# Performance work log

Hardware: AMD Instinct MI355X
Metric: run time of the kernel (lower is better)

The kernel has to match this reference:

```python
import jax, jax.numpy as jnp
import numpy as np
from jax import lax

# Conv4d decomposed (as in the torch implementation) into a sum of Conv3d's
# over the first spatial kernel axis. Each 3D conv is vectorized by folding
# the strided first-dim slices into the batch dimension.

def conv4d(x, w, b, stride=(2, 2, 2, 2), padding=(1, 1, 1, 1)):
    # x: [B, Ci, D1, D2, D3, D4]; w: [Co, Ci, K1, K2, K3, K4]; b: [Co]
    B, Ci, D1, D2, D3, D4 = x.shape
    Co, _, K1, K2, K3, K4 = w.shape
    s1, p1 = stride[0], padding[0]
    T = (D1 + 2 * p1 - K1) // s1 + 1  # output size along first spatial dim
    xp = jnp.pad(x, ((0, 0), (0, 0), (p1, p1), (0, 0), (0, 0), (0, 0)))
    pad3 = [(padding[j], padding[j]) for j in (1, 2, 3)]
    out = None
    for i in range(K1):  # small fixed loop over kernel taps along dim0
        xi = xp[:, :, i:i + s1 * (T - 1) + 1:s1]           # [B, Ci, T, D2, D3, D4]
        xi = jnp.moveaxis(xi, 2, 1).reshape(B * T, Ci, D2, D3, D4)
        yi = lax.conv_general_dilated(
            xi, w[:, :, i], window_strides=stride[1:], padding=pad3,
            dimension_numbers=('NCDHW', 'OIDHW', 'NCDHW'))
        out = yi if out is None else out + yi
    O2, O3, O4 = out.shape[2], out.shape[3], out.shape[4]
    out = out.reshape(B, T, Co, O2, O3, O4)
    out = jnp.moveaxis(out, 1, 2)                          # [B, Co, T, O2, O3, O4]
    return out + b[None, :, None, None, None, None]


def setup_inputs() -> dict:
    key = jax.random.key(0)
    k0, k1, k2, k3, k4 = jax.random.split(key, 5)
    C, R = 16, 4  # in_channel, mlp_ratio
    H = C * R     # 64
    x = jax.random.normal(k0, (1, C, 32, 32, 32, 32), dtype=jnp.float32)
    w1 = jax.random.normal(k1, (H, C, 3, 3, 3, 3), dtype=jnp.float32) * 0.02
    b1 = jax.random.normal(k2, (H,), dtype=jnp.float32) * 0.02
    w2 = jax.random.normal(k3, (C, H, 3, 3, 3, 3), dtype=jnp.float32) * 0.02
    b2 = jax.random.normal(k4, (C,), dtype=jnp.float32) * 0.02
    return {'x': x, 'w1': w1, 'b1': b1, 'w2': w2, 'b2': b2}


def reference(x, w1, b1, w2, b2):
    h = conv4d(x, w1, b1)                      # [1, 64, 16, 16, 16, 16]
    h = jax.nn.gelu(h, approximate=False)      # exact erf GELU (torch default)
    return conv4d(h, w2, b2)                   # [1, 16, 8, 8, 8, 8]
```

## Files before the change

kernel.cpp:

```cpp
#include <hip/hip_runtime.h>
#include <hip/hip_bf16.h>
#include <math.h>


typedef __attribute__((ext_vector_type(8))) short short8;
typedef __attribute__((ext_vector_type(4))) float f32x4;
typedef __attribute__((ext_vector_type(4))) unsigned int uint4v;

__device__ __forceinline__ unsigned short f2bf(float v) {
    __hip_bfloat16 b = __float2bfloat16(v);
    return *(unsigned short*)&b;
}

__global__ void setup_kernel(const float* __restrict__ w1, const float* __restrict__ w2,
                             const float* __restrict__ b2,
                             unsigned short* __restrict__ w1p, unsigned short* __restrict__ w2p,
                             uint4v* __restrict__ hz, float* __restrict__ out) {
    int b = blockIdx.x, tid = threadIdx.x;
    if (b < 544) {
        int i = b * 256 + tid;
        int kp = i % 136, co = (i / 136) & 63, ci = i / 8704;
        float v = 0.f;
        if (kp < 108 && (kp & 3) < 3) v = w1[(co * 16 + ci) * 81 + (kp >> 2) * 3 + (kp & 3)];
        w1p[i] = f2bf(v);
    } else if (b < 1088) {
        int i = (b - 544) * 256 + tid;
        int kp = i % 136, co = (i / 136) & 15, ci = i / 2176;
        float v = 0.f;
        if (kp < 108 && (kp & 3) < 3) v = w2[(co * 64 + ci) * 81 + (kp >> 2) * 3 + (kp & 3)];
        w2p[i] = f2bf(v);
    } else if (b < 1344) {
        int i = (b - 1088) * 256 + tid;
        out[i] = b2[i >> 12];
    } else {
        int i = (b - 1344) * 256 + tid;
        hz[i] = (uint4v){0, 0, 0, 0};
        int j = i + 704512;
        if (j < 839808) hz[j] = (uint4v){0, 0, 0, 0};
    }
}

__global__ __launch_bounds__(256) void conv1_mfma(
        const float* __restrict__ x, const unsigned short* __restrict__ w1p,
        const float* __restrict__ b1, unsigned short* __restrict__ hpad) {
    __shared__ unsigned short sX[36000];

    const int tid = threadIdx.x;
    const int bid = blockIdx.x;
    const int t4 = bid & 1, t3 = (bid >> 1) & 7, t2 = (bid >> 4) & 7, t1 = bid >> 7;
    const int bo1 = 2 * t1, bo2 = 2 * t2, bo3 = 2 * t3, bo4 = 8 * t4;
    const int g1b = 2 * bo1 - 1, g2b = 2 * bo2 - 1, g3b = 2 * bo3 - 1, g4b = 2 * bo4 - 1;

    int offs[5], swb[5];
    unsigned mka = 0, mkb = 0;
#pragma unroll
    for (int r = 0; r < 5; ++r) {
        int u = tid + 256 * r;
        bool uok = u < 1125;
        int uu = uok ? u : 0;
        int p = uu % 9, q = uu / 9;
        int i3 = q % 5; q /= 5;
        int i2 = q % 5; int i1 = q / 5;
        int g1 = g1b + i1, g2 = g2b + i2, g3 = g3b + i3;
        bool ok123 = uok & ((unsigned)g1 < 32u) & ((unsigned)g2 < 32u) & ((unsigned)g3 < 32u);
        int g4a = g4b + 2 * p;
        offs[r] = ((g1 * 32 + g2) * 32 + g3) * 32 + g4a;
        if (ok123 && (unsigned)g4a < 32u) mka |= 1u << r;
        if (ok123 && (unsigned)(g4a + 1) < 32u) mkb |= 1u << r;
        swb[r] = 2 * (((i1 * 5 + i2) * 5 + i3) * 18 + 2 * p);
    }

    auto gatherX = [&](int ci, float (&a)[5], float (&b)[5]) {
        const float* xc = x + (size_t)ci * 1048576;
#pragma unroll
        for (int r = 0; r < 5; ++r) {
            float va = 0.f, vb = 0.f;
            if ((mka >> r) & 1) va = xc[offs[r]];
            if ((mkb >> r) & 1) vb = xc[offs[r] + 1];
            a[r] = va; b[r] = vb;
        }
    };
    auto writeSlab = [&](int ci, const float (&a)[5], const float (&b)[5]) {
        char* slab = (char*)sX + ci * 4500;
#pragma unroll
        for (int r = 0; r < 4; ++r)
            *(unsigned*)(slab + swb[r]) = (unsigned)f2bf(a[r]) | ((unsigned)f2bf(b[r]) << 16);
        if (tid < 101)
            *(unsigned*)(slab + swb[4]) = (unsigned)f2bf(a[4]) | ((unsigned)f2bf(b[4]) << 16);
    };

    {
        float a0[5], b0[5], a1[5], b1v[5];
        gatherX(0, a0, b0);
        gatherX(1, a1, b1v);
        for (int cc = 0; cc < 16; cc += 2) {
            writeSlab(cc, a0, b0);
            if (cc + 2 < 16) gatherX(cc + 2, a0, b0);
            writeSlab(cc + 1, a1, b1v);
            if (cc + 3 < 16) gatherX(cc + 3, a1, b1v);
        }
    }
    __syncthreads();

    const int lane = tid & 63, wv = tid >> 6;
    const int n16 = lane & 15, hi = lane >> 4;
    const int ct0 = 2 * (wv & 1);
    const int st0 = 2 * (wv >> 1);

    int fpb[2];
#pragma unroll
    for (int tt = 0; tt < 2; ++tt) {
        int sp = (st0 + tt) * 16 + n16;
        int o4l = sp & 7, o3l = (sp >> 3) & 1, o2l = (sp >> 4) & 1, o1l = sp >> 5;
        fpb[tt] = 2 * (900 * o1l + 180 * o2l + 36 * o3l + 2 * o4l);
    }
    int kof[4][2];
#pragma unroll
    for (int ks = 0; ks < 4; ++ks)
#pragma unroll
    for (int j = 0; j < 2; ++j) {
        int g = 8 * ks + 2 * hi + j;
        if (g > 26) g = 26;
        int k1 = g / 9, k2 = (g / 3) % 3, k3 = g % 3;
        kof[ks][j] = 2 * (450 * k1 + 90 * k2 + 18 * k3);
    }

    auto loadA = [&](int ci, short8 (&Ac)[8]) {
        const unsigned short* aw0 = w1p + (size_t)(ci * 64 + 16 * ct0 + n16) * 136 + hi * 8;
#pragma unroll
        for (int k = 0; k < 4; ++k) Ac[k] = *(const short8*)(aw0 + 32 * k);
        const unsigned short* aw1 = aw0 + 16 * 136;
#pragma unroll
        for (int k = 0; k < 4; ++k) Ac[4 + k] = *(const short8*)(aw1 + 32 * k);
    };
    auto readFR = [&](int ci, short8 (&fr)[2][4]) {
        const char* sx = (const char*)sX + ci * 4500;
#pragma unroll
        for (int tt = 0; tt < 2; ++tt) {
            const char* base = sx + fpb[tt];
#pragma unroll
            for (int ks = 0; ks < 4; ++ks) {
                unsigned r0 = *(const unsigned*)(base + kof[ks][0]);
                unsigned r1 = *(const unsigned*)(base + kof[ks][0] + 4);
                unsigned r2 = *(const unsigned*)(base + kof[ks][1]);
                unsigned r3 = *(const unsigned*)(base + kof[ks][1] + 4);
                uint4v t = (uint4v){r0, r1, r2, r3};
                fr[tt][ks] = *(short8*)&t;
            }
        }
    };

    f32x4 acc[2][2];
#pragma unroll
    for (int c = 0; c < 2; ++c)
#pragma unroll
    for (int t = 0; t < 2; ++t) acc[c][t] = (f32x4){0.f, 0.f, 0.f, 0.f};

    auto mfma16 = [&](const short8 (&Ac)[8], const short8 (&fr)[2][4]) {
        __builtin_amdgcn_s_setprio(1);
#pragma unroll
        for (int tt = 0; tt < 2; ++tt)
#pragma unroll
        for (int ks = 0; ks < 4; ++ks) {
            acc[0][tt] = __builtin_amdgcn_mfma_f32_16x16x32_bf16(Ac[ks],     fr[tt][ks], acc[0][tt], 0, 0, 0);
            acc[1][tt] = __builtin_amdgcn_mfma_f32_16x16x32_bf16(Ac[4 + ks], fr[tt][ks], acc[1][tt], 0, 0, 0);
        }
        __builtin_amdgcn_s_setprio(0);
    };

    short8 A0[8], A1[8], F0[2][4], F1[2][4];
    loadA(0, A0);
    loadA(1, A1);
    readFR(0, F0);

    for (int cc = 0; cc < 16; cc += 2) {
        readFR(cc + 1, F1);
        mfma16(A0, F0);
        if (cc < 14) { loadA(cc + 2, A0); readFR(cc + 2, F0); }
        mfma16(A1, F1);
        if (cc < 14) loadA(cc + 3, A1);
    }

#pragma unroll
    for (int c = 0; c < 2; ++c) {
#pragma unroll
        for (int tt = 0; tt < 2; ++tt) {
            int spl = 16 * (st0 + tt) + n16;
            int e4 = spl & 7, e3 = (spl >> 3) & 1, e2 = (spl >> 4) & 1, e1 = spl >> 5;
            size_t base = (size_t)(bo1 + e1 + 1) * 5832 + (bo2 + e2 + 1) * 324 +
                          (bo3 + e3 + 1) * 18 + (bo4 + e4 + 1);
#pragma unroll
            for (int r = 0; r < 4; ++r) {
                int co = 16 * (ct0 + c) + 4 * hi + r;
                float v = acc[c][tt][r] + b1[co];
                v = 0.5f * v * (1.f + erff(v * 0.70710678118654752f));
                hpad[(size_t)co * 104976 + base] = f2bf(v);
            }
        }
    }
}

__global__ __launch_bounds__(256) void conv2_mfma(
        const unsigned short* __restrict__ hpad, const unsigned short* __restrict__ w2p,
        float* __restrict__ out) {
    __shared__ unsigned short sX[18000];

    const int tid = threadIdx.x;
    const int bid = blockIdx.x;
    const int s = bid & 63, cig = bid >> 6;
    const int t3 = s & 3, t2 = (s >> 2) & 3, t1 = s >> 4;
    const int bo1 = 2 * t1, bo2 = 2 * t2, bo3 = 2 * t3;

    int offs[5], swb[5];
#pragma unroll
    for (int r = 0; r < 5; ++r) {
        int u = tid + 256 * r;
        if (u >= 1125) u = 0;
        int p = u % 9, q = u / 9;
        int i3 = q % 5; q /= 5;
        int i2 = q % 5; int i1 = q / 5;
        offs[r] = (2 * bo1 + i1) * 5832 + (2 * bo2 + i2) * 324 + (2 * bo3 + i3) * 18 + 2 * p;
        swb[r] = 2 * (((i1 * 5 + i2) * 5 + i3) * 18 + 2 * p);
    }

    {
        unsigned fa[5], na[5];
        const unsigned short* h0 = hpad + (size_t)(cig * 8) * 104976;
#pragma unroll
        for (int r = 0; r < 5; ++r) fa[r] = *(const unsigned*)(h0 + offs[r]);
        for (int s8 = 0; s8 < 8; ++s8) {
            if (s8 < 7) {
                const unsigned short* hc = hpad + (size_t)(cig * 8 + s8 + 1) * 104976;
#pragma unroll
                for (int r = 0; r < 5; ++r) na[r] = *(const unsigned*)(hc + offs[r]);
            }
            char* slab = (char*)sX + s8 * 4500;
#pragma unroll
            for (int r = 0; r < 4; ++r) *(unsigned*)(slab + swb[r]) = fa[r];
            if (tid < 101) *(unsigned*)(slab + swb[4]) = fa[4];
            if (s8 < 7) {
#pragma unroll
                for (int r = 0; r < 5; ++r) fa[r] = na[r];
            }
        }
    }
    __syncthreads();

    const int lane = tid & 63, wv = tid >> 6;
    const int n16 = lane & 15, hi = lane >> 4;

    int fpb;
    {
        int sp = wv * 16 + n16;
        int o4l = sp & 7, o3l = (sp >> 3) & 1, o2l = (sp >> 4) & 1, o1l = sp >> 5;
        fpb = 2 * (900 * o1l + 180 * o2l + 36 * o3l + 2 * o4l);
    }
    int kof[4][2];
#pragma unroll
    for (int ks = 0; ks < 4; ++ks)
#pragma unroll
    for (int j = 0; j < 2; ++j) {
        int g = 8 * ks + 2 * hi + j;
        if (g > 26) g = 26;
        int k1 = g / 9, k2 = (g / 3) % 3, k3 = g % 3;
        kof[ks][j] = 2 * (450 * k1 + 90 * k2 + 18 * k3);
    }

    auto loadA = [&](int s8, short8 (&Ac)[4]) {
        const unsigned short* aw = w2p + (size_t)((cig * 8 + s8) * 16 + n16) * 136 + hi * 8;
#pragma unroll
        for (int k = 0; k < 4; ++k) Ac[k] = *(const short8*)(aw + 32 * k);
    };
    auto readFR = [&](int s8, short8 (&fr)[4]) {
        const char* base = (const char*)sX + s8 * 4500 + fpb;
#pragma unroll
        for (int ks = 0; ks < 4; ++ks) {
            unsigned r0 = *(const unsigned*)(base + kof[ks][0]);
            unsigned r1 = *(const unsigned*)(base + kof[ks][0] + 4);
            unsigned r2 = *(const unsigned*)(base + kof[ks][1]);
            unsigned r3 = *(const unsigned*)(base + kof[ks][1] + 4);
            uint4v tmp = (uint4v){r0, r1, r2, r3};
            fr[ks] = *(short8*)&tmp;
        }
    };

    f32x4 acc = (f32x4){0.f, 0.f, 0.f, 0.f};
    short8 A0[4], A1[4], F0[4], F1[4];
    loadA(0, A0);
    loadA(1, A1);
    readFR(0, F0);

    auto mfma4 = [&](const short8 (&Ac)[4], const short8 (&fr)[4]) {
        __builtin_amdgcn_s_setprio(1);
#pragma unroll
        for (int ks = 0; ks < 4; ++ks)
            acc = __builtin_amdgcn_mfma_f32_16x16x32_bf16(Ac[ks], fr[ks], acc, 0, 0, 0);
        __builtin_amdgcn_s_setprio(0);
    };

    for (int cc = 0; cc < 8; cc += 2) {
        readFR(cc + 1, F1);
        mfma4(A0, F0);
        if (cc < 6) { loadA(cc + 2, A0); readFR(cc + 2, F0); }
        mfma4(A1, F1);
        if (cc < 6) loadA(cc + 3, A1);
    }

    {
        int spl = 16 * wv + n16;
        int e4 = spl & 7, e3 = (spl >> 3) & 1, e2 = (spl >> 4) & 1, e1 = spl >> 5;
        int o1 = bo1 + e1, o2 = bo2 + e2, o3 = bo3 + e3, o4 = e4;
#pragma unroll
        for (int r = 0; r < 4; ++r) {
            int co = 4 * hi + r;
            atomicAdd(&out[(size_t)co * 4096 + o1 * 512 + o2 * 64 + o3 * 8 + o4], acc[r]);
        }
    }
}

extern "C" void kernel_launch(void* const* d_in, const int* in_sizes, int n_in,
                              void* d_out, int out_size, void* d_ws, size_t ws_size,
                              hipStream_t stream) {
    const float* x  = (const float*)d_in[0];
    const float* w1 = (const float*)d_in[1];
    const float* b1 = (const float*)d_in[2];
    const float* w2 = (const float*)d_in[3];
    const float* b2 = (const float*)d_in[4];
    float* out = (float*)d_out;

    unsigned short* hpad = (unsigned short*)d_ws;
    unsigned short* w1p  = hpad + 6718464;
    unsigned short* w2p  = w1p + 139264;

    setup_kernel<<<4096, 256, 0, stream>>>(w1, w2, b2, w1p, w2p, (uint4v*)hpad, out);
    conv1_mfma<<<1024, 256, 0, stream>>>(x, w1p, b1, hpad);
    conv2_mfma<<<512, 256, 0, stream>>>(hpad, w2p, out);
}
```

Before: 85.98 us.

## Pre-pad input to bf16 buffer and load conv1 B-fragments directly from global

Adds a kernel that converts x to a zero-padded bf16 tensor in workspace, then conv1 drops its LDS staging slab and gathers B fragments straight from global memory with precomputed offsets, pipelined with the weight loads. This removes the shared-memory gather/convert phase, the barrier and the LDS footprint, which may raise occupancy. In exchange it adds an extra kernel launch and a full read and write of the padded input, and the fragment loads become scattered 8-byte global reads that rely on cache reuse.

```diff
diff --git a/kernel.cpp b/kernel.cpp
--- a/kernel.cpp
+++ b/kernel.cpp
@@ -6,6 +6,7 @@
 typedef __attribute__((ext_vector_type(8))) short short8;
 typedef __attribute__((ext_vector_type(4))) float f32x4;
 typedef __attribute__((ext_vector_type(4))) unsigned int uint4v;
+typedef unsigned uint2a __attribute__((ext_vector_type(2), aligned(4)));
 
 __device__ __forceinline__ unsigned short f2bf(float v) {
     __hip_bfloat16 b = __float2bfloat16(v);
@@ -40,91 +41,64 @@
     }
 }
 
+__global__ void build_xpad(const float* __restrict__ x, unsigned short* __restrict__ xp) {
+    const int N = 16 * 34 * 34 * 34 * 34;
+    for (int i = blockIdx.x * 256 + threadIdx.x; i < N; i += 16384 * 256) {
+        int u = i;
+        int g4 = u % 34; u /= 34;
+        int g3 = u % 34; u /= 34;
+        int g2 = u % 34; u /= 34;
+        int g1 = u % 34; int ci = u / 34;
+        float v = 0.f;
+        if ((unsigned)(g1 - 1) < 32u && (unsigned)(g2 - 1) < 32u &&
+            (unsigned)(g3 - 1) < 32u && (unsigned)(g4 - 1) < 32u)
+            v = x[((((ci * 32 + g1 - 1) * 32 + g2 - 1) * 32 + g3 - 1) << 5) + g4 - 1];
+        xp[i] = f2bf(v);
+    }
+}
+
 __global__ __launch_bounds__(256) void conv1_mfma(
-        const float* __restrict__ x, const unsigned short* __restrict__ w1p,
+        const unsigned short* __restrict__ xp, const unsigned short* __restrict__ w1p,
         const float* __restrict__ b1, unsigned short* __restrict__ hpad) {
-    __shared__ unsigned short sX[36000];
-
     const int tid = threadIdx.x;
     const int bid = blockIdx.x;
     const int t4 = bid & 1, t3 = (bid >> 1) & 7, t2 = (bid >> 4) & 7, t1 = bid >> 7;
     const int bo1 = 2 * t1, bo2 = 2 * t2, bo3 = 2 * t3, bo4 = 8 * t4;
-    const int g1b = 2 * bo1 - 1, g2b = 2 * bo2 - 1, g3b = 2 * bo3 - 1, g4b = 2 * bo4 - 1;
-
-    int offs[5], swb[5];
-    unsigned mka = 0, mkb = 0;
-#pragma unroll
-    for (int r = 0; r < 5; ++r) {
-        int u = tid + 256 * r;
-        bool uok = u < 1125;
-        int uu = uok ? u : 0;
-        int p = uu % 9, q = uu / 9;
-        int i3 = q % 5; q /= 5;
-        int i2 = q % 5; int i1 = q / 5;
-        int g1 = g1b + i1, g2 = g2b + i2, g3 = g3b + i3;
-        bool ok123 = uok & ((unsigned)g1 < 32u) & ((unsigned)g2 < 32u) & ((unsigned)g3 < 32u);
-        int g4a = g4b + 2 * p;
-        offs[r] = ((g1 * 32 + g2) * 32 + g3) * 32 + g4a;
-        if (ok123 && (unsigned)g4a < 32u) mka |= 1u << r;
-        if (ok123 && (unsigned)(g4a + 1) < 32u) mkb |= 1u << r;
-        swb[r] = 2 * (((i1 * 5 + i2) * 5 + i3) * 18 + 2 * p);
-    }
-
-    auto gatherX = [&](int ci, float (&a)[5], float (&b)[5]) {
-        const float* xc = x + (size_t)ci * 1048576;
-#pragma unroll
-        for (int r = 0; r < 5; ++r) {
-            float va = 0.f, vb = 0.f;
-            if ((mka >> r) & 1) va = xc[offs[r]];
-            if ((mkb >> r) & 1) vb = xc[offs[r] + 1];
-            a[r] = va; b[r] = vb;
-        }
-    };
-    auto writeSlab = [&](int ci, const float (&a)[5], const float (&b)[5]) {
-        char* slab = (char*)sX + ci * 4500;
-#pragma unroll
-        for (int r = 0; r < 4; ++r)
-            *(unsigned*)(slab + swb[r]) = (unsigned)f2bf(a[r]) | ((unsigned)f2bf(b[r]) << 16);
-        if (tid < 101)
-            *(unsigned*)(slab + swb[4]) = (unsigned)f2bf(a[4]) | ((unsigned)f2bf(b[4]) << 16);
-    };
-
-    {
-        float a0[5], b0[5], a1[5], b1v[5];
-        gatherX(0, a0, b0);
-        gatherX(1, a1, b1v);
-        for (int cc = 0; cc < 16; cc += 2) {
-            writeSlab(cc, a0, b0);
-            if (cc + 2 < 16) gatherX(cc + 2, a0, b0);
-            writeSlab(cc + 1, a1, b1v);
-            if (cc + 3 < 16) gatherX(cc + 3, a1, b1v);
-        }
-    }
-    __syncthreads();
 
     const int lane = tid & 63, wv = tid >> 6;
     const int n16 = lane & 15, hi = lane >> 4;
     const int ct0 = 2 * (wv & 1);
     const int st0 = 2 * (wv >> 1);
 
-    int fpb[2];
+    int boff[2][4][2];
 #pragma unroll
     for (int tt = 0; tt < 2; ++tt) {
-        int sp = (st0 + tt) * 16 + n16;
-        int o4l = sp & 7, o3l = (sp >> 3) & 1, o2l = (sp >> 4) & 1, o1l = sp >> 5;
-        fpb[tt] = 2 * (900 * o1l + 180 * o2l + 36 * o3l + 2 * o4l);
-    }
-    int kof[4][2];
-#pragma unroll
-    for (int ks = 0; ks < 4; ++ks)
-#pragma unroll
-    for (int j = 0; j < 2; ++j) {
-        int g = 8 * ks + 2 * hi + j;
-        if (g > 26) g = 26;
-        int k1 = g / 9, k2 = (g / 3) % 3, k3 = g % 3;
-        kof[ks][j] = 2 * (450 * k1 + 90 * k2 + 18 * k3);
-    }
-
+        int spl = (st0 + tt) * 16 + n16;
+        int o4l = spl & 7, o3l = (spl >> 3) & 1, o2l = (spl >> 4) & 1, o1l = spl >> 5;
+        int G1 = 2 * (bo1 + o1l), G2 = 2 * (bo2 + o2l), G3 = 2 * (bo3 + o3l), G4 = 2 * (bo4 + o4l);
+#pragma unroll
+        for (int ks = 0; ks < 4; ++ks)
+#pragma unroll
+        for (int j = 0; j < 2; ++j) {
+            int g = 8 * ks + 2 * hi + j;
+            if (g > 26) g = 26;
+            int k1 = g / 9, k2 = (g / 3) % 3, k3 = g % 3;
+            boff[tt][ks][j] = 2 * ((((G1 + k1) * 34 + G2 + k2) * 34 + G3 + k3) * 34 + G4);
+        }
+    }
+
+    auto loadB = [&](int ci, short8 (&F)[2][4]) {
+        const char* base = (const char*)xp + (size_t)ci * 2672672;
+#pragma unroll
+        for (int tt = 0; tt < 2; ++tt)
+#pragma unroll
+        for (int ks = 0; ks < 4; ++ks) {
+            uint2a v0 = *(const uint2a*)(base + boff[tt][ks][0]);
+            uint2a v1 = *(const uint2a*)(base + boff[tt][ks][1]);
+            uint4v t = (uint4v){v0.x, v0.y, v1.x, v1.y};
+            F[tt][ks] = *(short8*)&t;
+        }
+    };
     auto loadA = [&](int ci, short8 (&Ac)[8]) {
         const unsigned short* aw0 = w1p + (size_t)(ci * 64 + 16 * ct0 + n16) * 136 + hi * 8;
 #pragma unroll
@@ -132,22 +106,6 @@
         const unsigned short* aw1 = aw0 + 16 * 136;
 #pragma unroll
         for (int k = 0; k < 4; ++k) Ac[4 + k] = *(const short8*)(aw1 + 32 * k);
-    };
-    auto readFR = [&](int ci, short8 (&fr)[2][4]) {
-        const char* sx = (const char*)sX + ci * 4500;
-#pragma unroll
-        for (int tt = 0; tt < 2; ++tt) {
-            const char* base = sx + fpb[tt];
-#pragma unroll
-            for (int ks = 0; ks < 4; ++ks) {
-                unsigned r0 = *(const unsigned*)(base + kof[ks][0]);
-                unsigned r1 = *(const unsigned*)(base + kof[ks][0] + 4);
-                unsigned r2 = *(const unsigned*)(base + kof[ks][1]);
-                unsigned r3 = *(const unsigned*)(base + kof[ks][1] + 4);
-                uint4v t = (uint4v){r0, r1, r2, r3};
-                fr[tt][ks] = *(short8*)&t;
-            }
-        }
     };
 
     f32x4 acc[2][2];
@@ -169,16 +127,14 @@
     };
 
     short8 A0[8], A1[8], F0[2][4], F1[2][4];
-    loadA(0, A0);
-    loadA(1, A1);
-    readFR(0, F0);
+    loadB(0, F0); loadA(0, A0);
+    loadB(1, F1); loadA(1, A1);
 
     for (int cc = 0; cc < 16; cc += 2) {
-        readFR(cc + 1, F1);
         mfma16(A0, F0);
-        if (cc < 14) { loadA(cc + 2, A0); readFR(cc + 2, F0); }
+        if (cc < 14) { loadB(cc + 2, F0); loadA(cc + 2, A0); }
         mfma16(A1, F1);
-        if (cc < 14) loadA(cc + 3, A1);
+        if (cc < 14) { loadB(cc + 3, F1); loadA(cc + 3, A1); }
     }
 
 #pragma unroll
@@ -331,8 +287,10 @@
     unsigned short* hpad = (unsigned short*)d_ws;
     unsigned short* w1p  = hpad + 6718464;
     unsigned short* w2p  = w1p + 139264;
+    unsigned short* xpad = w2p + 139264;
 
     setup_kernel<<<4096, 256, 0, stream>>>(w1, w2, b2, w1p, w2p, (uint4v*)hpad, out);
-    conv1_mfma<<<1024, 256, 0, stream>>>(x, w1p, b1, hpad);
+    build_xpad<<<16384, 256, 0, stream>>>(x, xpad);
+    conv1_mfma<<<1024, 256, 0, stream>>>(xpad, w1p, b1, hpad);
     conv2_mfma<<<512, 256, 0, stream>>>(hpad, w2p, out);
 }
```

After: 121.3 us. 1.41x slower.
